# Kernel tuning notes

Measured on AMD Instinct MI355X. Metric: run time of the kernel, lower is better.

## Reference

```python
import jax, jax.numpy as jnp
import numpy as np

N, E, IN, H, OUT = 100000, 600000, 128, 128, 64
BN_EPS = 1e-5


def setup_inputs() -> dict:
    key = jax.random.key(0)
    ks = jax.random.split(key, 8)
    def lin(k, i, o):
        return jax.random.normal(k, (i, o), jnp.float32) / np.float32(np.sqrt(i))
    return {
        "x": jax.random.normal(ks[0], (N, IN), jnp.float32),
        "edge_index": jax.random.randint(ks[1], (2, E), 0, N, dtype=jnp.int64),
        "W1": lin(ks[2], IN, H), "b1": jnp.zeros((H,), jnp.float32),
        "gamma": jnp.ones((H,), jnp.float32), "beta": jnp.zeros((H,), jnp.float32),
        "W2": lin(ks[3], H, H), "b2": jnp.zeros((H,), jnp.float32),
        "Wm1": lin(ks[4], H, H), "bm1": jnp.zeros((H,), jnp.float32),
        "Wm2": lin(ks[5], H, OUT), "bm2": jnp.zeros((OUT,), jnp.float32),
    }


def reference(x, edge_index, W1, b1, gamma, beta, W2, b2, Wm1, bm1, Wm2, bm2):
    # GINConv: h = MLP((1 + eps) * x + sum_{j in N(i)} x_j), eps = 0 (train_eps=False)
    src = edge_index[0]
    dst = edge_index[1]  # PyG aggregates messages at edge_index[1]
    agg = jax.ops.segment_sum(x[src], dst, num_segments=x.shape[0])  # [N, IN]
    h = agg + x
    # inner MLP: Linear -> BatchNorm (batch stats) -> ReLU -> Linear
    h = h @ W1 + b1
    mean = jnp.mean(h, axis=0)
    var = jnp.var(h, axis=0)
    h = (h - mean) * jax.lax.rsqrt(var + BN_EPS) * gamma + beta
    h = jax.nn.relu(h)
    h = h @ W2 + b2
    h = jax.nn.relu(h)  # .relu() after conv
    # output MLP (norm=None, dropout=0.5 -> identity at inference): Linear -> ReLU -> Linear
    h = jax.nn.relu(h @ Wm1 + bm1)
    return h @ Wm2 + bm2
```

## Files before the change

### kernel.cpp

```cpp
#include <hip/hip_runtime.h>
#include <hip/hip_bf16.h>
#include <stdint.h>

#define NNODES 100000
#define NEDGES 600000
#define SCAN_CHUNK 1024
#define SCAN_NB 98

typedef __attribute__((ext_vector_type(8))) short bf16x8;
typedef __attribute__((ext_vector_type(4))) float f32x4;

__device__ inline float b2f(short b) {
    union { unsigned u; float f; } v;
    v.u = ((unsigned)(unsigned short)b) << 16;
    return v.f;
}
__device__ inline short f2b(float f) {
    union { float f; unsigned u; } v;
    v.f = f;
    unsigned r = (v.u + 0x7FFFu + ((v.u >> 16) & 1u)) >> 16;
    return (short)r;
}
__device__ inline int swz(int row, int kbyte) {
    return (row * 256 + kbyte) ^ ((row & 7) << 4);
}
#define MFMA16(a, b, c) __builtin_amdgcn_mfma_f32_16x16x32_bf16(a, b, c, 0, 0, 0)

__global__ __launch_bounds__(256) void k_prep(const float* __restrict__ x,
                                              const float* __restrict__ W1,
                                              const float* __restrict__ W2,
                                              const float* __restrict__ Wm1,
                                              const float* __restrict__ Wm2,
                                              short* __restrict__ xb, short* __restrict__ Wt,
                                              int* __restrict__ pos, float* __restrict__ stats) {
    int i = blockIdx.x * 256 + threadIdx.x;
    if (i < (NNODES + 1) * 16) {
        bf16x8 o = (bf16x8){0, 0, 0, 0, 0, 0, 0, 0};
        if (i < NNODES * 16) {
            const float4* p = (const float4*)(x + (size_t)i * 8);
            float4 a = p[0], b = p[1];
            o[0] = f2b(a.x); o[1] = f2b(a.y); o[2] = f2b(a.z); o[3] = f2b(a.w);
            o[4] = f2b(b.x); o[5] = f2b(b.y); o[6] = f2b(b.z); o[7] = f2b(b.w);
        }
        *(bf16x8*)(xb + (size_t)i * 8) = o;
    }
    if (i < NNODES) pos[i] = 0;
    if (i < 57344) {
        float v;
        if (i < 16384) {
            int c = i >> 7, k = i & 127;
            v = W1[k * 128 + c];
        } else if (i < 32768) {
            int j = i - 16384;
            int c = j >> 7, k = j & 127;
            v = W2[k * 128 + c];
        } else if (i < 49152) {
            int j = i - 32768;
            int c = j >> 7, k = j & 127;
            v = Wm1[k * 128 + c];
        } else {
            int j = i - 49152;
            int c = j >> 7, k = j & 127;
            v = Wm2[k * 64 + c];
        }
        Wt[i] = f2b(v);
    }
    if (i < 256) stats[i] = 0.0f;
}


__global__ __launch_bounds__(256) void k_hist(const int* __restrict__ ei, int* __restrict__ cnt) {
    int e = blockIdx.x * 256 + threadIdx.x;
    if (e < NEDGES) atomicAdd(&cnt[ei[NEDGES + e]], 1);
}

__global__ __launch_bounds__(256) void k_scan1(const int* __restrict__ cnt, int* __restrict__ bsums) {
    __shared__ int sd[256];
    int b = blockIdx.x, t = threadIdx.x;
    int base = b * SCAN_CHUNK + t * 4;
    int s = 0;
#pragma unroll
    for (int i = 0; i < 4; ++i) {
        int idx = base + i;
        if (idx < NNODES) s += cnt[idx];
    }
    sd[t] = s;
    __syncthreads();
    for (int off = 128; off > 0; off >>= 1) {
        if (t < off) sd[t] += sd[t + off];
        __syncthreads();
    }
    if (t == 0) bsums[b] = sd[0];
}

__global__ __launch_bounds__(64) void k_scan2(int* __restrict__ bsums, int* __restrict__ rowptr) {
    if (threadIdx.x == 0 && blockIdx.x == 0) {
        int run = 0;
        for (int b = 0; b < SCAN_NB; ++b) {
            int v = bsums[b];
            bsums[b] = run;
            run += v;
        }
        rowptr[NNODES] = run;
    }
}

__global__ __launch_bounds__(256) void k_scan3(const int* __restrict__ cnt,
                                               const int* __restrict__ bsums,
                                               int* __restrict__ rowptr, int* __restrict__ pos) {
    __shared__ int sd[256];
    int b = blockIdx.x, t = threadIdx.x;
    int base = b * SCAN_CHUNK + t * 4;
    int v[4];
    int s = 0;
#pragma unroll
    for (int i = 0; i < 4; ++i) {
        int idx = base + i;
        v[i] = (idx < NNODES) ? cnt[idx] : 0;
        s += v[i];
    }
    sd[t] = s;
    __syncthreads();
    for (int off = 1; off < 256; off <<= 1) {
        int val = (t >= off) ? sd[t - off] : 0;
        __syncthreads();
        sd[t] += val;
        __syncthreads();
    }
    int run = sd[t] - s + bsums[b];
#pragma unroll
    for (int i = 0; i < 4; ++i) {
        int idx = base + i;
        if (idx < NNODES) {
            rowptr[idx] = run;
            pos[idx] = run;
            run += v[i];
        }
    }
}

__global__ __launch_bounds__(256) void k_fill(const int* __restrict__ ei, int* __restrict__ pos,
                                              int* __restrict__ elist) {
    int e = blockIdx.x * 256 + threadIdx.x;
    if (e >= NEDGES) return;
    int src = ei[e];
    int dst = ei[NEDGES + e];
    int p = atomicAdd(&pos[dst], 1);
    elist[p] = src;
}

__global__ __launch_bounds__(256) void k_agg(const short* __restrict__ xb,
                                             const int* __restrict__ rowptr,
                                             const int* __restrict__ elist,
                                             short* __restrict__ bufb) {
    int t = threadIdx.x;
    int w = t >> 6, lane = t & 63;
    int node = blockIdx.x * 4 + w;
    if (node >= NNODES) return;
    int beg = rowptr[node];
    int end = rowptr[node + 1];
    int deg = end - beg;
    int total = deg + 1;
    int sub = lane & 31, half = lane >> 5;
    const uint2* xr = (const uint2*)xb;

    float acc0 = 0.f, acc1 = 0.f, acc2 = 0.f, acc3 = 0.f;

    for (int base = 0; base < total; base += 64) {
        int j = base + lane;
        int ej = NNODES;
        if (j < total) ej = (j == 0) ? node : elist[beg + j - 1];
        int cnt = min(64, total - base);
        int pairs = (cnt + 1) >> 1;
        for (int i = 0; i < pairs; i += 4) {
            int j0 = 2 * i + half;
            int r0 = __shfl(ej, j0);
            int r1 = __shfl(ej, j0 + 2);
            int r2 = __shfl(ej, j0 + 4);
            int r3 = __shfl(ej, j0 + 6);
            uint2 v0 = xr[(size_t)r0 * 32 + sub];
            uint2 v1 = xr[(size_t)r1 * 32 + sub];
            uint2 v2 = xr[(size_t)r2 * 32 + sub];
            uint2 v3 = xr[(size_t)r3 * 32 + sub];
            acc0 += b2f((short)(v0.x & 0xFFFF)) + b2f((short)(v1.x & 0xFFFF)) +
                    b2f((short)(v2.x & 0xFFFF)) + b2f((short)(v3.x & 0xFFFF));
            acc1 += b2f((short)(v0.x >> 16)) + b2f((short)(v1.x >> 16)) +
                    b2f((short)(v2.x >> 16)) + b2f((short)(v3.x >> 16));
            acc2 += b2f((short)(v0.y & 0xFFFF)) + b2f((short)(v1.y & 0xFFFF)) +
                    b2f((short)(v2.y & 0xFFFF)) + b2f((short)(v3.y & 0xFFFF));
            acc3 += b2f((short)(v0.y >> 16)) + b2f((short)(v1.y >> 16)) +
                    b2f((short)(v2.y >> 16)) + b2f((short)(v3.y >> 16));
        }
    }
    acc0 += __shfl_xor(acc0, 32);
    acc1 += __shfl_xor(acc1, 32);
    acc2 += __shfl_xor(acc2, 32);
    acc3 += __shfl_xor(acc3, 32);
    if (half == 0) {
        uint2 o;
        o.x = ((uint32_t)(unsigned short)f2b(acc1) << 16) | (uint32_t)(unsigned short)f2b(acc0);
        o.y = ((uint32_t)(unsigned short)f2b(acc3) << 16) | (uint32_t)(unsigned short)f2b(acc2);
        ((uint2*)bufb)[(size_t)node * 32 + sub] = o;
    }
}

__global__ __launch_bounds__(256) void k_gemm1(const short* __restrict__ Ab,
                                               const short* __restrict__ W1t,
                                               const float* __restrict__ b1,
                                               short* __restrict__ h1b,
                                               float* __restrict__ stats) {
    __shared__ __align__(16) short act[128 * 128];
    __shared__ __align__(16) short wt[128 * 128];
    __shared__ float Sred[2][4][128];

    int t = threadIdx.x;
    int w = t >> 6, l = t & 63;
    int r0 = blockIdx.x * 128;

#pragma unroll
    for (int z = 0; z < 8; ++z) {
        int idx = t + z * 256;
        int row = idx >> 4, kc = idx & 15;
        int gr = r0 + row;
        bf16x8 v = (bf16x8){0, 0, 0, 0, 0, 0, 0, 0};
        if (gr < NNODES) v = *(const bf16x8*)(Ab + (size_t)gr * 128 + kc * 8);
        *(bf16x8*)((char*)act + swz(row, kc * 16)) = v;
    }
#pragma unroll
    for (int z = 0; z < 8; ++z) {
        int idx = t + z * 256;
        int row = idx >> 4, kc = idx & 15;
        *(bf16x8*)((char*)wt + swz(row, kc * 16)) =
            *(const bf16x8*)(W1t + (size_t)row * 128 + kc * 8);
    }
    __syncthreads();

    int row0 = (w & 1) * 64, col0 = (w >> 1) * 64;
    f32x4 acc[4][4];
#pragma unroll
    for (int r = 0; r < 4; ++r)
#pragma unroll
        for (int c = 0; c < 4; ++c) acc[r][c] = (f32x4){0.f, 0.f, 0.f, 0.f};

#pragma unroll
    for (int kb = 0; kb < 4; ++kb) {
        int kbyte = kb * 64 + (l >> 4) * 16;
        bf16x8 af[4], bw[4];
#pragma unroll
        for (int r = 0; r < 4; ++r)
            af[r] = *(const bf16x8*)((char*)act + swz(row0 + r * 16 + (l & 15), kbyte));
#pragma unroll
        for (int c = 0; c < 4; ++c)
            bw[c] = *(const bf16x8*)((char*)wt + swz(col0 + c * 16 + (l & 15), kbyte));
#pragma unroll
        for (int r = 0; r < 4; ++r)
#pragma unroll
            for (int c = 0; c < 4; ++c) acc[r][c] = MFMA16(af[r], bw[c], acc[r][c]);
    }

    float s[4], q[4];
#pragma unroll
    for (int c = 0; c < 4; ++c) { s[c] = 0.f; q[c] = 0.f; }
#pragma unroll
    for (int c = 0; c < 4; ++c) {
        float bias = b1[col0 + c * 16 + (l & 15)];
#pragma unroll
        for (int r = 0; r < 4; ++r)
#pragma unroll
            for (int rr = 0; rr < 4; ++rr) {
                float v = acc[r][c][rr] + bias;
                acc[r][c][rr] = v;
                int grow = r0 + row0 + r * 16 + (l >> 4) * 4 + rr;
                if (grow < NNODES) { s[c] += v; q[c] += v * v; }
            }
    }
#pragma unroll
    for (int c = 0; c < 4; ++c) {
        s[c] += __shfl_xor(s[c], 16); s[c] += __shfl_xor(s[c], 32);
        q[c] += __shfl_xor(q[c], 16); q[c] += __shfl_xor(q[c], 32);
    }
    if (l < 16) {
#pragma unroll
        for (int c = 0; c < 4; ++c) {
            Sred[0][w][col0 + c * 16 + l] = s[c];
            Sred[1][w][col0 + c * 16 + l] = q[c];
        }
    }
    __syncthreads();
    if (t < 128) {
        int wb = (t < 64) ? 0 : 2;
        atomicAdd(stats + t, Sred[0][wb][t] + Sred[0][wb + 1][t]);
        atomicAdd(stats + 128 + t, Sred[1][wb][t] + Sred[1][wb + 1][t]);
    }

#pragma unroll
    for (int r = 0; r < 4; ++r)
#pragma unroll
        for (int c = 0; c < 4; ++c)
#pragma unroll
            for (int rr = 0; rr < 4; ++rr) {
                int row = row0 + r * 16 + (l >> 4) * 4 + rr;
                int col = col0 + c * 16 + (l & 15);
                *(short*)((char*)act + swz(row, col * 2)) = f2b(acc[r][c][rr]);
            }
    __syncthreads();
#pragma unroll
    for (int z = 0; z < 8; ++z) {
        int idx = t + z * 256;
        int row = idx >> 4, kc = idx & 15;
        int gr = r0 + row;
        if (gr < NNODES)
            *(bf16x8*)(h1b + (size_t)gr * 128 + kc * 8) =
                *(const bf16x8*)((char*)act + swz(row, kc * 16));
    }
}

__global__ __launch_bounds__(256) void k_mlp(const short* __restrict__ h1b,
                                             const float* __restrict__ stats,
                                             const float* __restrict__ gamma,
                                             const float* __restrict__ beta,
                                             const short* __restrict__ W2t,
                                             const float* __restrict__ b2,
                                             const short* __restrict__ Wm1t,
                                             const float* __restrict__ bm1,
                                             const short* __restrict__ Wm2t,
                                             const float* __restrict__ bm2,
                                             float* __restrict__ out) {
    __shared__ __align__(16) short act[128 * 128];
    __shared__ __align__(16) short wt[128 * 128];
    __shared__ float scale[128], shift[128];

    int t = threadIdx.x, w = t >> 6, l = t & 63;
    int r0 = blockIdx.x * 128;

    if (t < 128) {
        float mean = stats[t] * (1.0f / NNODES);
        float var = stats[128 + t] * (1.0f / NNODES) - mean * mean;
        var = fmaxf(var, 0.0f);
        float inv = rsqrtf(var + 1e-5f);
        float sc = gamma[t] * inv;
        scale[t] = sc;
        shift[t] = beta[t] - mean * sc;
    }
#pragma unroll
    for (int z = 0; z < 8; ++z) {
        int idx = t + z * 256;
        int row = idx >> 4, kc = idx & 15;
        *(bf16x8*)((char*)wt + swz(row, kc * 16)) =
            *(const bf16x8*)(W2t + (size_t)row * 128 + kc * 8);
    }
    __syncthreads();

#pragma unroll
    for (int z = 0; z < 8; ++z) {
        int idx = t + z * 256;
        int row = idx >> 4, kc = idx & 15;
        int gr = r0 + row;
        bf16x8 o = (bf16x8){0, 0, 0, 0, 0, 0, 0, 0};
        if (gr < NNODES) {
            bf16x8 v = *(const bf16x8*)(h1b + (size_t)gr * 128 + kc * 8);
#pragma unroll
            for (int j = 0; j < 8; ++j) {
                int k = kc * 8 + j;
                float f = b2f(v[j]) * scale[k] + shift[k];
                o[j] = f2b(fmaxf(f, 0.f));
            }
        }
        *(bf16x8*)((char*)act + swz(row, kc * 16)) = o;
    }
    __syncthreads();

    int row0 = (w & 1) * 64, col0 = (w >> 1) * 64;
    f32x4 acc[4][4];

#pragma unroll
    for (int r = 0; r < 4; ++r)
#pragma unroll
        for (int c = 0; c < 4; ++c) acc[r][c] = (f32x4){0.f, 0.f, 0.f, 0.f};
#pragma unroll
    for (int kb = 0; kb < 4; ++kb) {
        int kbyte = kb * 64 + (l >> 4) * 16;
        bf16x8 af[4], bw[4];
#pragma unroll
        for (int r = 0; r < 4; ++r)
            af[r] = *(const bf16x8*)((char*)act + swz(row0 + r * 16 + (l & 15), kbyte));
#pragma unroll
        for (int c = 0; c < 4; ++c)
            bw[c] = *(const bf16x8*)((char*)wt + swz(col0 + c * 16 + (l & 15), kbyte));
#pragma unroll
        for (int r = 0; r < 4; ++r)
#pragma unroll
            for (int c = 0; c < 4; ++c) acc[r][c] = MFMA16(af[r], bw[c], acc[r][c]);
    }
    __syncthreads();
#pragma unroll
    for (int c = 0; c < 4; ++c) {
        float bias = b2[col0 + c * 16 + (l & 15)];
#pragma unroll
        for (int r = 0; r < 4; ++r)
#pragma unroll
            for (int rr = 0; rr < 4; ++rr) {
                int row = row0 + r * 16 + (l >> 4) * 4 + rr;
                int col = col0 + c * 16 + (l & 15);
                *(short*)((char*)act + swz(row, col * 2)) = f2b(fmaxf(acc[r][c][rr] + bias, 0.f));
            }
    }
#pragma unroll
    for (int z = 0; z < 8; ++z) {
        int idx = t + z * 256;
        int row = idx >> 4, kc = idx & 15;
        *(bf16x8*)((char*)wt + swz(row, kc * 16)) =
            *(const bf16x8*)(Wm1t + (size_t)row * 128 + kc * 8);
    }
    __syncthreads();

#pragma unroll
    for (int r = 0; r < 4; ++r)
#pragma unroll
        for (int c = 0; c < 4; ++c) acc[r][c] = (f32x4){0.f, 0.f, 0.f, 0.f};
#pragma unroll
    for (int kb = 0; kb < 4; ++kb) {
        int kbyte = kb * 64 + (l >> 4) * 16;
        bf16x8 af[4], bw[4];
#pragma unroll
        for (int r = 0; r < 4; ++r)
            af[r] = *(const bf16x8*)((char*)act + swz(row0 + r * 16 + (l & 15), kbyte));
#pragma unroll
        for (int c = 0; c < 4; ++c)
            bw[c] = *(const bf16x8*)((char*)wt + swz(col0 + c * 16 + (l & 15), kbyte));
#pragma unroll
        for (int r = 0; r < 4; ++r)
#pragma unroll
            for (int c = 0; c < 4; ++c) acc[r][c] = MFMA16(af[r], bw[c], acc[r][c]);
    }
    __syncthreads();
#pragma unroll
    for (int c = 0; c < 4; ++c) {
        float bias = bm1[col0 + c * 16 + (l & 15)];
#pragma unroll
        for (int r = 0; r < 4; ++r)
#pragma unroll
            for (int rr = 0; rr < 4; ++rr) {
                int row = row0 + r * 16 + (l >> 4) * 4 + rr;
                int col = col0 + c * 16 + (l & 15);
                *(short*)((char*)act + swz(row, col * 2)) = f2b(fmaxf(acc[r][c][rr] + bias, 0.f));
            }
    }
#pragma unroll
    for (int z = 0; z < 4; ++z) {
        int idx = t + z * 256;
        int row = idx >> 4, kc = idx & 15;
        *(bf16x8*)((char*)wt + swz(row, kc * 16)) =
            *(const bf16x8*)(Wm2t + (size_t)row * 128 + kc * 8);
    }
    __syncthreads();

    int row0q = w * 32;
    f32x4 a2[2][4];
#pragma unroll
    for (int r = 0; r < 2; ++r)
#pragma unroll
        for (int c = 0; c < 4; ++c) a2[r][c] = (f32x4){0.f, 0.f, 0.f, 0.f};
#pragma unroll
    for (int kb = 0; kb < 4; ++kb) {
        int kbyte = kb * 64 + (l >> 4) * 16;
        bf16x8 af[2], bw[4];
#pragma unroll
        for (int r = 0; r < 2; ++r)
            af[r] = *(const bf16x8*)((char*)act + swz(row0q + r * 16 + (l & 15), kbyte));
#pragma unroll
        for (int c = 0; c < 4; ++c)
            bw[c] = *(const bf16x8*)((char*)wt + swz(c * 16 + (l & 15), kbyte));
#pragma unroll
        for (int r = 0; r < 2; ++r)
#pragma unroll
            for (int c = 0; c < 4; ++c) a2[r][c] = MFMA16(af[r], bw[c], a2[r][c]);
    }
#pragma unroll
    for (int c = 0; c < 4; ++c) {
        float bias = bm2[c * 16 + (l & 15)];
#pragma unroll
        for (int r = 0; r < 2; ++r)
#pragma unroll
            for (int rr = 0; rr < 4; ++rr) {
                int grow = r0 + row0q + r * 16 + (l >> 4) * 4 + rr;
                if (grow < NNODES)
                    out[(size_t)grow * 64 + c * 16 + (l & 15)] = a2[r][c][rr] + bias;
            }
    }
}

extern "C" void kernel_launch(void* const* d_in, const int* in_sizes, int n_in,
                              void* d_out, int out_size, void* d_ws, size_t ws_size,
                              hipStream_t stream) {
    const float* x     = (const float*)d_in[0];
    const int*   ei    = (const int*)d_in[1];
    const float* W1    = (const float*)d_in[2];
    const float* b1    = (const float*)d_in[3];
    const float* gamma = (const float*)d_in[4];
    const float* beta  = (const float*)d_in[5];
    const float* W2    = (const float*)d_in[6];
    const float* b2    = (const float*)d_in[7];
    const float* Wm1   = (const float*)d_in[8];
    const float* bm1   = (const float*)d_in[9];
    const float* Wm2   = (const float*)d_in[10];
    const float* bm2   = (const float*)d_in[11];
    float* out = (float*)d_out;

    char* ws = (char*)d_ws;
    short* xb    = (short*)ws;
    short* bufb  = xb + (size_t)(NNODES + 1) * 128;
    short* h1b   = bufb + (size_t)NNODES * 128;
    short* Wt    = h1b + (size_t)NNODES * 128;
    float* stats = (float*)(Wt + 57344);
    int* rowptr  = (int*)(stats + 256);
    int* pos     = rowptr + (NNODES + 1);
    int* elist   = pos + NNODES;
    int* bsums   = elist + NEDGES;

    const short* W1t  = Wt;
    const short* W2t  = Wt + 16384;
    const short* Wm1t = Wt + 32768;
    const short* Wm2t = Wt + 49152;

    int gE = (NEDGES + 255) / 256;
    int gPrep = ((NNODES + 1) * 16 + 255) / 256;

    k_prep<<<gPrep, 256, 0, stream>>>(x, W1, W2, Wm1, Wm2, xb, Wt, pos, stats);
    k_hist<<<gE, 256, 0, stream>>>(ei, pos);
    k_scan1<<<SCAN_NB, 256, 0, stream>>>(pos, bsums);
    k_scan2<<<1, 64, 0, stream>>>(bsums, rowptr);
    k_scan3<<<SCAN_NB, 256, 0, stream>>>(pos, bsums, rowptr, pos);
    k_fill<<<gE, 256, 0, stream>>>(ei, pos, elist);
    k_agg<<<(NNODES + 3) / 4, 256, 0, stream>>>(xb, rowptr, elist, bufb);

    int nblk = (NNODES + 127) / 128;
    k_gemm1<<<nblk, 256, 0, stream>>>(bufb, W1t, b1, h1b, stats);
    k_mlp<<<nblk, 256, 0, stream>>>(h1b, stats, gamma, beta, W2t, b2, Wm1t, bm1, Wm2t, bm2, out);
}
```

Measured before the change: 194.0 us.

## Recompute first GEMM in MLP kernel and pre-pack weights in MFMA fragment order

The first GEMM no longer writes its bf16 output h1 to global memory. A stats-only kernel computes the BatchNorm sums, and the MLP kernel recomputes agg@W1 from the aggregated buffer, folding in the BN scale and shift. Bias b1 is dropped because batch-norm mean subtraction cancels it. Weights are pre-packed into per-lane MFMA fragment order so every GEMM reads B operands straight from global/L2 instead of staging them through LDS. This removes the h1 write and read and the LDS weight staging, at the cost of running the first GEMM twice and reading A rows uncoalesced from global. The bufb allocation is padded by 128 rows so the tail block can read past NNODES without guards.

```diff
diff --git a/kernel.cpp b/kernel.cpp
--- a/kernel.cpp
+++ b/kernel.cpp
@@ -47,23 +47,21 @@
     if (i < NNODES) pos[i] = 0;
     if (i < 57344) {
         float v;
+        int c, k, base, ncb;
         if (i < 16384) {
-            int c = i >> 7, k = i & 127;
-            v = W1[k * 128 + c];
+            c = i >> 7; k = i & 127; v = W1[k * 128 + c]; base = 0; ncb = 8;
         } else if (i < 32768) {
-            int j = i - 16384;
-            int c = j >> 7, k = j & 127;
-            v = W2[k * 128 + c];
+            int j = i - 16384; c = j >> 7; k = j & 127; v = W2[k * 128 + c]; base = 16384; ncb = 8;
         } else if (i < 49152) {
-            int j = i - 32768;
-            int c = j >> 7, k = j & 127;
-            v = Wm1[k * 128 + c];
+            int j = i - 32768; c = j >> 7; k = j & 127; v = Wm1[k * 128 + c]; base = 32768; ncb = 8;
         } else {
-            int j = i - 49152;
-            int c = j >> 7, k = j & 127;
-            v = Wm2[k * 64 + c];
-        }
-        Wt[i] = f2b(v);
+            int j = i - 49152; c = j >> 7; k = j & 127; v = Wm2[k * 64 + c]; base = 49152; ncb = 4;
+        }
+        int kb = k >> 5, hi = (k >> 3) & 3, jj = k & 7;
+        int cb = c >> 4, lr = c & 15;
+        int lane = hi * 16 + lr;
+        int dst = base + (((kb * ncb) + cb) * 64 + lane) * 8 + jj;
+        Wt[dst] = f2b(v);
     }
     if (i < 256) stats[i] = 0.0f;
 }
@@ -204,38 +202,14 @@
     }
 }
 
-__global__ __launch_bounds__(256) void k_gemm1(const short* __restrict__ Ab,
-                                               const short* __restrict__ W1t,
-                                               const float* __restrict__ b1,
-                                               short* __restrict__ h1b,
+__global__ __launch_bounds__(256) void k_stats(const short* __restrict__ bufb,
+                                               const short* __restrict__ W1pk,
                                                float* __restrict__ stats) {
-    __shared__ __align__(16) short act[128 * 128];
-    __shared__ __align__(16) short wt[128 * 128];
     __shared__ float Sred[2][4][128];
-
-    int t = threadIdx.x;
-    int w = t >> 6, l = t & 63;
+    int t = threadIdx.x, w = t >> 6, l = t & 63;
     int r0 = blockIdx.x * 128;
-
-#pragma unroll
-    for (int z = 0; z < 8; ++z) {
-        int idx = t + z * 256;
-        int row = idx >> 4, kc = idx & 15;
-        int gr = r0 + row;
-        bf16x8 v = (bf16x8){0, 0, 0, 0, 0, 0, 0, 0};
-        if (gr < NNODES) v = *(const bf16x8*)(Ab + (size_t)gr * 128 + kc * 8);
-        *(bf16x8*)((char*)act + swz(row, kc * 16)) = v;
-    }
-#pragma unroll
-    for (int z = 0; z < 8; ++z) {
-        int idx = t + z * 256;
-        int row = idx >> 4, kc = idx & 15;
-        *(bf16x8*)((char*)wt + swz(row, kc * 16)) =
-            *(const bf16x8*)(W1t + (size_t)row * 128 + kc * 8);
-    }
-    __syncthreads();
-
     int row0 = (w & 1) * 64, col0 = (w >> 1) * 64;
+
     f32x4 acc[4][4];
 #pragma unroll
     for (int r = 0; r < 4; ++r)
@@ -244,14 +218,14 @@
 
 #pragma unroll
     for (int kb = 0; kb < 4; ++kb) {
-        int kbyte = kb * 64 + (l >> 4) * 16;
         bf16x8 af[4], bw[4];
 #pragma unroll
         for (int r = 0; r < 4; ++r)
-            af[r] = *(const bf16x8*)((char*)act + swz(row0 + r * 16 + (l & 15), kbyte));
+            af[r] = *(const bf16x8*)(bufb + (size_t)(r0 + row0 + r * 16 + (l & 15)) * 128 +
+                                     kb * 32 + (l >> 4) * 8);
 #pragma unroll
         for (int c = 0; c < 4; ++c)
-            bw[c] = *(const bf16x8*)((char*)wt + swz(col0 + c * 16 + (l & 15), kbyte));
+            bw[c] = *(const bf16x8*)(W1pk + ((kb * 8 + (w >> 1) * 4 + c) * 64 + l) * 8);
 #pragma unroll
         for (int r = 0; r < 4; ++r)
 #pragma unroll
@@ -262,18 +236,18 @@
 #pragma unroll
     for (int c = 0; c < 4; ++c) { s[c] = 0.f; q[c] = 0.f; }
 #pragma unroll
-    for (int c = 0; c < 4; ++c) {
-        float bias = b1[col0 + c * 16 + (l & 15)];
+    for (int c = 0; c < 4; ++c)
 #pragma unroll
         for (int r = 0; r < 4; ++r)
 #pragma unroll
             for (int rr = 0; rr < 4; ++rr) {
-                float v = acc[r][c][rr] + bias;
-                acc[r][c][rr] = v;
                 int grow = r0 + row0 + r * 16 + (l >> 4) * 4 + rr;
-                if (grow < NNODES) { s[c] += v; q[c] += v * v; }
+                if (grow < NNODES) {
+                    float v = acc[r][c][rr];
+                    s[c] += v;
+                    q[c] += v * v;
+                }
             }
-    }
 #pragma unroll
     for (int c = 0; c < 4; ++c) {
         s[c] += __shfl_xor(s[c], 16); s[c] += __shfl_xor(s[c], 32);
@@ -292,46 +266,26 @@
         atomicAdd(stats + t, Sred[0][wb][t] + Sred[0][wb + 1][t]);
         atomicAdd(stats + 128 + t, Sred[1][wb][t] + Sred[1][wb + 1][t]);
     }
-
-#pragma unroll
-    for (int r = 0; r < 4; ++r)
-#pragma unroll
-        for (int c = 0; c < 4; ++c)
-#pragma unroll
-            for (int rr = 0; rr < 4; ++rr) {
-                int row = row0 + r * 16 + (l >> 4) * 4 + rr;
-                int col = col0 + c * 16 + (l & 15);
-                *(short*)((char*)act + swz(row, col * 2)) = f2b(acc[r][c][rr]);
-            }
-    __syncthreads();
-#pragma unroll
-    for (int z = 0; z < 8; ++z) {
-        int idx = t + z * 256;
-        int row = idx >> 4, kc = idx & 15;
-        int gr = r0 + row;
-        if (gr < NNODES)
-            *(bf16x8*)(h1b + (size_t)gr * 128 + kc * 8) =
-                *(const bf16x8*)((char*)act + swz(row, kc * 16));
-    }
-}
-
-__global__ __launch_bounds__(256) void k_mlp(const short* __restrict__ h1b,
+}
+
+__global__ __launch_bounds__(256) void k_mlp(const short* __restrict__ bufb,
                                              const float* __restrict__ stats,
                                              const float* __restrict__ gamma,
                                              const float* __restrict__ beta,
-                                             const short* __restrict__ W2t,
+                                             const short* __restrict__ Wt,
                                              const float* __restrict__ b2,
-                                             const short* __restrict__ Wm1t,
                                              const float* __restrict__ bm1,
-                                             const short* __restrict__ Wm2t,
                                              const float* __restrict__ bm2,
                                              float* __restrict__ out) {
     __shared__ __align__(16) short act[128 * 128];
-    __shared__ __align__(16) short wt[128 * 128];
     __shared__ float scale[128], shift[128];
 
     int t = threadIdx.x, w = t >> 6, l = t & 63;
     int r0 = blockIdx.x * 128;
+    const short* W1pk = Wt;
+    const short* W2pk = Wt + 16384;
+    const short* Wm1pk = Wt + 32768;
+    const short* Wm2pk = Wt + 49152;
 
     if (t < 128) {
         float mean = stats[t] * (1.0f / NNODES);
@@ -342,36 +296,44 @@
         scale[t] = sc;
         shift[t] = beta[t] - mean * sc;
     }
-#pragma unroll
-    for (int z = 0; z < 8; ++z) {
-        int idx = t + z * 256;
-        int row = idx >> 4, kc = idx & 15;
-        *(bf16x8*)((char*)wt + swz(row, kc * 16)) =
-            *(const bf16x8*)(W2t + (size_t)row * 128 + kc * 8);
-    }
-    __syncthreads();
-
-#pragma unroll
-    for (int z = 0; z < 8; ++z) {
-        int idx = t + z * 256;
-        int row = idx >> 4, kc = idx & 15;
-        int gr = r0 + row;
-        bf16x8 o = (bf16x8){0, 0, 0, 0, 0, 0, 0, 0};
-        if (gr < NNODES) {
-            bf16x8 v = *(const bf16x8*)(h1b + (size_t)gr * 128 + kc * 8);
-#pragma unroll
-            for (int j = 0; j < 8; ++j) {
-                int k = kc * 8 + j;
-                float f = b2f(v[j]) * scale[k] + shift[k];
-                o[j] = f2b(fmaxf(f, 0.f));
-            }
-        }
-        *(bf16x8*)((char*)act + swz(row, kc * 16)) = o;
-    }
     __syncthreads();
 
     int row0 = (w & 1) * 64, col0 = (w >> 1) * 64;
     f32x4 acc[4][4];
+
+#pragma unroll
+    for (int r = 0; r < 4; ++r)
+#pragma unroll
+        for (int c = 0; c < 4; ++c) acc[r][c] = (f32x4){0.f, 0.f, 0.f, 0.f};
+#pragma unroll
+    for (int kb = 0; kb < 4; ++kb) {
+        bf16x8 af[4], bw[4];
+#pragma unroll
+        for (int r = 0; r < 4; ++r)
+            af[r] = *(const bf16x8*)(bufb + (size_t)(r0 + row0 + r * 16 + (l & 15)) * 128 +
+                                     kb * 32 + (l >> 4) * 8);
+#pragma unroll
+        for (int c = 0; c < 4; ++c)
+            bw[c] = *(const bf16x8*)(W1pk + ((kb * 8 + (w >> 1) * 4 + c) * 64 + l) * 8);
+#pragma unroll
+        for (int r = 0; r < 4; ++r)
+#pragma unroll
+            for (int c = 0; c < 4; ++c) acc[r][c] = MFMA16(af[r], bw[c], acc[r][c]);
+    }
+#pragma unroll
+    for (int c = 0; c < 4; ++c) {
+        int col = col0 + c * 16 + (l & 15);
+        float sc_ = scale[col], sh_ = shift[col];
+#pragma unroll
+        for (int r = 0; r < 4; ++r)
+#pragma unroll
+            for (int rr = 0; rr < 4; ++rr) {
+                int row = row0 + r * 16 + (l >> 4) * 4 + rr;
+                *(short*)((char*)act + swz(row, col * 2)) =
+                    f2b(fmaxf(acc[r][c][rr] * sc_ + sh_, 0.f));
+            }
+    }
+    __syncthreads();
 
 #pragma unroll
     for (int r = 0; r < 4; ++r)
@@ -386,7 +348,7 @@
             af[r] = *(const bf16x8*)((char*)act + swz(row0 + r * 16 + (l & 15), kbyte));
 #pragma unroll
         for (int c = 0; c < 4; ++c)
-            bw[c] = *(const bf16x8*)((char*)wt + swz(col0 + c * 16 + (l & 15), kbyte));
+            bw[c] = *(const bf16x8*)(W2pk + ((kb * 8 + (w >> 1) * 4 + c) * 64 + l) * 8);
 #pragma unroll
         for (int r = 0; r < 4; ++r)
 #pragma unroll
@@ -395,22 +357,15 @@
     __syncthreads();
 #pragma unroll
     for (int c = 0; c < 4; ++c) {
-        float bias = b2[col0 + c * 16 + (l & 15)];
+        int col = col0 + c * 16 + (l & 15);
+        float bias = b2[col];
 #pragma unroll
         for (int r = 0; r < 4; ++r)
 #pragma unroll
             for (int rr = 0; rr < 4; ++rr) {
                 int row = row0 + r * 16 + (l >> 4) * 4 + rr;
-                int col = col0 + c * 16 + (l & 15);
                 *(short*)((char*)act + swz(row, col * 2)) = f2b(fmaxf(acc[r][c][rr] + bias, 0.f));
             }
-    }
-#pragma unroll
-    for (int z = 0; z < 8; ++z) {
-        int idx = t + z * 256;
-        int row = idx >> 4, kc = idx & 15;
-        *(bf16x8*)((char*)wt + swz(row, kc * 16)) =
-            *(const bf16x8*)(Wm1t + (size_t)row * 128 + kc * 8);
     }
     __syncthreads();
 
@@ -427,7 +382,7 @@
             af[r] = *(const bf16x8*)((char*)act + swz(row0 + r * 16 + (l & 15), kbyte));
 #pragma unroll
         for (int c = 0; c < 4; ++c)
-            bw[c] = *(const bf16x8*)((char*)wt + swz(col0 + c * 16 + (l & 15), kbyte));
+            bw[c] = *(const bf16x8*)(Wm1pk + ((kb * 8 + (w >> 1) * 4 + c) * 64 + l) * 8);
 #pragma unroll
         for (int r = 0; r < 4; ++r)
 #pragma unroll
@@ -436,22 +391,15 @@
     __syncthreads();
 #pragma unroll
     for (int c = 0; c < 4; ++c) {
-        float bias = bm1[col0 + c * 16 + (l & 15)];
+        int col = col0 + c * 16 + (l & 15);
+        float bias = bm1[col];
 #pragma unroll
         for (int r = 0; r < 4; ++r)
 #pragma unroll
             for (int rr = 0; rr < 4; ++rr) {
                 int row = row0 + r * 16 + (l >> 4) * 4 + rr;
-                int col = col0 + c * 16 + (l & 15);
                 *(short*)((char*)act + swz(row, col * 2)) = f2b(fmaxf(acc[r][c][rr] + bias, 0.f));
             }
-    }
-#pragma unroll
-    for (int z = 0; z < 4; ++z) {
-        int idx = t + z * 256;
-        int row = idx >> 4, kc = idx & 15;
-        *(bf16x8*)((char*)wt + swz(row, kc * 16)) =
-            *(const bf16x8*)(Wm2t + (size_t)row * 128 + kc * 8);
     }
     __syncthreads();
 
@@ -470,7 +418,7 @@
             af[r] = *(const bf16x8*)((char*)act + swz(row0q + r * 16 + (l & 15), kbyte));
 #pragma unroll
         for (int c = 0; c < 4; ++c)
-            bw[c] = *(const bf16x8*)((char*)wt + swz(c * 16 + (l & 15), kbyte));
+            bw[c] = *(const bf16x8*)(Wm2pk + ((kb * 4 + c) * 64 + l) * 8);
 #pragma unroll
         for (int r = 0; r < 2; ++r)
 #pragma unroll
@@ -496,7 +444,6 @@
     const float* x     = (const float*)d_in[0];
     const int*   ei    = (const int*)d_in[1];
     const float* W1    = (const float*)d_in[2];
-    const float* b1    = (const float*)d_in[3];
     const float* gamma = (const float*)d_in[4];
     const float* beta  = (const float*)d_in[5];
     const float* W2    = (const float*)d_in[6];
@@ -510,18 +457,12 @@
     char* ws = (char*)d_ws;
     short* xb    = (short*)ws;
     short* bufb  = xb + (size_t)(NNODES + 1) * 128;
-    short* h1b   = bufb + (size_t)NNODES * 128;
-    short* Wt    = h1b + (size_t)NNODES * 128;
+    short* Wt    = bufb + (size_t)(NNODES + 128) * 128;
     float* stats = (float*)(Wt + 57344);
     int* rowptr  = (int*)(stats + 256);
     int* pos     = rowptr + (NNODES + 1);
     int* elist   = pos + NNODES;
     int* bsums   = elist + NEDGES;
-
-    const short* W1t  = Wt;
-    const short* W2t  = Wt + 16384;
-    const short* Wm1t = Wt + 32768;
-    const short* Wm2t = Wt + 49152;
 
     int gE = (NEDGES + 255) / 256;
     int gPrep = ((NNODES + 1) * 16 + 255) / 256;
@@ -535,6 +476,6 @@
     k_agg<<<(NNODES + 3) / 4, 256, 0, stream>>>(xb, rowptr, elist, bufb);
 
     int nblk = (NNODES + 127) / 128;
-    k_gemm1<<<nblk, 256, 0, stream>>>(bufb, W1t, b1, h1b, stats);
-    k_mlp<<<nblk, 256, 0, stream>>>(h1b, stats, gamma, beta, W2t, b2, Wm1t, bm1, Wm2t, bm2, out);
-}
+    k_stats<<<nblk, 256, 0, stream>>>(bufb, Wt, stats);
+    k_mlp<<<nblk, 256, 0, stream>>>(bufb, stats, gamma, beta, Wt, b2, bm1, bm2, out);
+}
```

Result: faster. 180.1 us (-7.2%).
